# Performance work log

Hardware: AMD Instinct MI355X
Metric: run time of the kernel (lower is better)

## Reference

```python
import jax, jax.numpy as jnp
import numpy as np

N = 10000        # nodes
E = 640000       # edges (before self-loops)
IN = 128         # in_channels
HID = 32         # hidden_channels
HEADS = 4
HC = HID * HEADS # 128
OUT = 40         # out_channels
NEG_SLOPE = 0.2  # PyG GATConv default


def setup_inputs() -> dict:
    key = jax.random.key(0)
    ks = jax.random.split(key, 12)
    g = lambda k, shape: (jax.random.normal(k, shape, jnp.float32) * 0.1)
    return {
        "x": jax.random.normal(ks[0], (N, IN), jnp.float32),
        "edge_index": jax.random.randint(ks[1], (2, E), 0, N, dtype=jnp.int32),
        # conv1: in -> HID per head, HEADS heads, concat
        "W1": g(ks[2], (IN, HEADS * HID)),
        "a_src1": g(ks[3], (HEADS, HID)),
        "a_dst1": g(ks[4], (HEADS, HID)),
        "b1": jnp.zeros((HEADS * HID,), jnp.float32),
        # conv2: HC -> HC, 1 head
        "W2": g(ks[5], (HC, HC)),
        "a_src2": g(ks[6], (1, HC)),
        "a_dst2": g(ks[7], (1, HC)),
        "b2": jnp.zeros((HC,), jnp.float32),
        # final linear head
        "Wlin": g(ks[8], (HC, OUT)),
        "blin": jnp.zeros((OUT,), jnp.float32),
    }


def _gat_layer(x, W, a_src, a_dst, b, src, dst, heads, n):
    """PyG-style GATConv: gather -> edge attention -> segment softmax -> scatter."""
    d = W.shape[1] // heads
    h = (x @ W).reshape(n, heads, d)                       # [N, H, d]
    asrc = jnp.einsum('nhd,hd->nh', h, a_src)              # [N, H]
    adst = jnp.einsum('nhd,hd->nh', h, a_dst)
    e = jax.nn.leaky_relu(asrc[src] + adst[dst], NEG_SLOPE)  # [E, H]
    m = jax.ops.segment_max(e, dst, num_segments=n)          # per-dst max (stable softmax)
    p = jnp.exp(e - m[dst])
    z = jax.ops.segment_sum(p, dst, num_segments=n)
    alpha = p / (z[dst] + 1e-16)                             # [E, H]
    out = jax.ops.segment_sum(h[src] * alpha[:, :, None], dst, num_segments=n)
    return out.reshape(n, heads * d) + b


def reference(x, edge_index, W1, a_src1, a_dst1, b1, W2, a_src2, a_dst2, b2, Wlin, blin):
    n = x.shape[0]
    loop = jnp.arange(n, dtype=edge_index.dtype)           # add_self_loops=True
    src = jnp.concatenate([edge_index[0], loop])
    dst = jnp.concatenate([edge_index[1], loop])
    # eval mode: dropout is identity
    h1 = jax.nn.elu(_gat_layer(x, W1, a_src1, a_dst1, b1, src, dst, HEADS, n))
    h2 = jax.nn.elu(_gat_layer(h1, W2, a_src2, a_dst2, b2, src, dst, 1, n))
    return h2 @ Wlin + blin
```

## Files before the change

kernel.cpp:

```cpp
#include <hip/hip_runtime.h>
#include <hip/hip_bf16.h>

#define KSUB 8
#define SUBCAP 32
#define CAP 256

using bf16x8 = __attribute__((ext_vector_type(8))) short;
using f32x4  = __attribute__((ext_vector_type(4))) float;

static __device__ __forceinline__ short f2b(float f) {
    __hip_bfloat16 h = __float2bfloat16(f);
    return *reinterpret_cast<short*>(&h);
}
static __device__ __forceinline__ float blo(unsigned u) { return __uint_as_float(u << 16); }
static __device__ __forceinline__ float bhi(unsigned u) { return __uint_as_float(u & 0xffff0000u); }

__global__ void build_csr(const int* __restrict__ srcArr, const int* __restrict__ dstArr,
                          int E, int N, int* __restrict__ deg2,
                          unsigned short* __restrict__ csr) {
    int tid = threadIdx.x;
    int k_sub = blockIdx.x & (KSUB - 1);
    int Etot = E + N;
    int base = blockIdx.x * 1024 + tid;
#pragma unroll
    for (int k = 0; k < 4; k++) {
        int i = base + k * 256;
        if (i < Etot) {
            int s, d;
            if (i < E) { s = srcArr[i]; d = dstArr[i]; }
            else       { s = d = i - E; }
            int p = atomicAdd(&deg2[d * KSUB + k_sub], 1);
            if (p < SUBCAP) csr[d * CAP + k_sub * SUBCAP + p] = (unsigned short)s;
        }
    }
}

__global__ __launch_bounds__(256) void prep_w(const float* __restrict__ W1,
                                              const float* __restrict__ W2,
                                              short* __restrict__ Wt1,
                                              short* __restrict__ Wt2) {
    __shared__ float t[32][33];
    int which = blockIdx.x >> 4;
    int tile = blockIdx.x & 15;
    int bi = tile >> 2, bj = tile & 3;
    const float* W = which ? W2 : W1;
    short* Wt = which ? Wt2 : Wt1;
    int tx = threadIdx.x & 31, ty = threadIdx.x >> 5;
#pragma unroll
    for (int i = 0; i < 4; i++) {
        int r = bi * 32 + ty + 8 * i;
        t[ty + 8 * i][tx] = W[r * 128 + bj * 32 + tx];
    }
    __syncthreads();
#pragma unroll
    for (int i = 0; i < 4; i++) {
        int j = bj * 32 + ty + 8 * i;
        Wt[j * 128 + bi * 32 + tx] = f2b(t[tx][ty + 8 * i]);
    }
}

template <int H>
__global__ __launch_bounds__(256) void gemm_mfma(const float* __restrict__ x,
                        const short* __restrict__ Wt,
                        const float* __restrict__ a_src, const float* __restrict__ a_dst,
                        __hip_bfloat16* __restrict__ hwb, float* __restrict__ asrc,
                        float* __restrict__ adst, int N) {
    int wave = (blockIdx.x * 256 + threadIdx.x) >> 6;
    int lane = threadIdx.x & 63;
    int n0 = wave * 16;
    if (n0 >= N) return;
    int m = lane & 15, q = lane >> 4;
    int row = n0 + m;
    bf16x8 afrag[4];
    const float* xr = x + (size_t)row * 128 + q * 8;
#pragma unroll
    for (int kt = 0; kt < 4; kt++) {
        float4 v0 = *(const float4*)(xr + kt * 32);
        float4 v1 = *(const float4*)(xr + kt * 32 + 4);
        bf16x8 f;
        f[0] = f2b(v0.x); f[1] = f2b(v0.y); f[2] = f2b(v0.z); f[3] = f2b(v0.w);
        f[4] = f2b(v1.x); f[5] = f2b(v1.y); f[6] = f2b(v1.z); f[7] = f2b(v1.w);
        afrag[kt] = f;
    }
    float vs[4] = {0.f, 0.f, 0.f, 0.f}, vd[4] = {0.f, 0.f, 0.f, 0.f};
#pragma unroll
    for (int ct = 0; ct < 8; ct++) {
        f32x4 acc = {0.f, 0.f, 0.f, 0.f};
        const short* wrow = Wt + (ct * 16 + m) * 128 + q * 8;
#pragma unroll
        for (int kt = 0; kt < 4; kt++) {
            bf16x8 bfrag = *(const bf16x8*)(wrow + kt * 32);
            acc = __builtin_amdgcn_mfma_f32_16x16x32_bf16(afrag[kt], bfrag, acc, 0, 0, 0);
        }
        int col = ct * 16 + m;
        float asv = a_src[col], adv = a_dst[col];
#pragma unroll
        for (int r = 0; r < 4; r++) {
            int rr = n0 + q * 4 + r;
            hwb[rr * 128 + col] = __float2bfloat16(acc[r]);
            vs[r] += acc[r] * asv;
            vd[r] += acc[r] * adv;
        }
        if (H == 4 && (ct & 1) == 1) {
#pragma unroll
            for (int r = 0; r < 4; r++) {
                float a = vs[r], d = vd[r];
                for (int off = 8; off >= 1; off >>= 1) {
                    a += __shfl_xor(a, off); d += __shfl_xor(d, off);
                }
                if (m == 0) {
                    int rr = n0 + q * 4 + r;
                    asrc[rr * 4 + (ct >> 1)] = a;
                    adst[rr * 4 + (ct >> 1)] = d;
                }
                vs[r] = 0.f; vd[r] = 0.f;
            }
        }
    }
    if (H == 1) {
#pragma unroll
        for (int r = 0; r < 4; r++) {
            float a = vs[r], d = vd[r];
            for (int off = 8; off >= 1; off >>= 1) {
                a += __shfl_xor(a, off); d += __shfl_xor(d, off);
            }
            if (m == 0) {
                int rr = n0 + q * 4 + r;
                asrc[rr] = a;
                adst[rr] = d;
            }
        }
    }
}

__device__ __forceinline__ int slot8(int idx, const int* pref) {
    int k = 0;
#pragma unroll
    for (int j = 1; j < KSUB; j++) k += (idx >= pref[j]);
    return k * SUBCAP + (idx - pref[k]);
}

__global__ __launch_bounds__(64) void agg4(const __hip_bfloat16* __restrict__ hw,
                     const float* __restrict__ asrc, const float* __restrict__ adst,
                     const int* __restrict__ deg2, const unsigned short* __restrict__ csr_src,
                     const float* __restrict__ b, float* __restrict__ y, int N) {
    int n = blockIdx.x;
    int t = threadIdx.x;
    int er = t >> 4;
    int cg = t & 15;
    int hcol = cg >> 2;
    const int4* dp = (const int4*)&deg2[n * KSUB];
    int4 ca = dp[0], cb2 = dp[1];
    int pref[KSUB];
    int cnts[KSUB] = { min(ca.x,SUBCAP), min(ca.y,SUBCAP), min(ca.z,SUBCAP), min(ca.w,SUBCAP),
                       min(cb2.x,SUBCAP), min(cb2.y,SUBCAP), min(cb2.z,SUBCAP), min(cb2.w,SUBCAP) };
    pref[0] = 0;
#pragma unroll
    for (int k = 1; k < KSUB; k++) pref[k] = pref[k-1] + cnts[k-1];
    int deg = pref[KSUB-1] + cnts[KSUB-1];
    const uint4* hw4 = (const uint4*)hw;
    __shared__ float pe[128 * 4];
    __shared__ int se[128];
    float4 adl = *(const float4*)&adst[n * 4];
    float acc[8] = {0.f,0.f,0.f,0.f,0.f,0.f,0.f,0.f};
    float z0 = 0.f, z1 = 0.f, z2 = 0.f, z3 = 0.f;
    for (int base = 0; base < deg; base += 128) {
        int cnt = min(128, deg - base);
        __syncthreads();
#pragma unroll
        for (int rep = 0; rep < 2; rep++) {
            int idx = t + 64 * rep;
            if (idx < cnt) {
                int s = (int)csr_src[n * CAP + slot8(base + idx, pref)];
                se[idx] = s;
                float4 av = *(const float4*)&asrc[s * 4];
                float e0 = av.x + adl.x, e1 = av.y + adl.y;
                float e2 = av.z + adl.z, e3 = av.w + adl.w;
                e0 = e0 > 0.f ? e0 : 0.2f * e0;
                e1 = e1 > 0.f ? e1 : 0.2f * e1;
                e2 = e2 > 0.f ? e2 : 0.2f * e2;
                e3 = e3 > 0.f ? e3 : 0.2f * e3;
                float p0 = __expf(e0), p1 = __expf(e1), p2 = __expf(e2), p3 = __expf(e3);
                pe[idx * 4 + 0] = p0; pe[idx * 4 + 1] = p1;
                pe[idx * 4 + 2] = p2; pe[idx * 4 + 3] = p3;
                z0 += p0; z1 += p1; z2 += p2; z3 += p3;
            }
        }
        __syncthreads();
        for (int c = er; c < cnt; c += 4) {
            int s = se[c];
            float p = pe[c * 4 + hcol];
            uint4 v = hw4[s * 16 + cg];
            acc[0] += p * blo(v.x); acc[1] += p * bhi(v.x);
            acc[2] += p * blo(v.y); acc[3] += p * bhi(v.y);
            acc[4] += p * blo(v.z); acc[5] += p * bhi(v.z);
            acc[6] += p * blo(v.w); acc[7] += p * bhi(v.w);
        }
    }
#pragma unroll
    for (int i = 0; i < 8; i++) {
        acc[i] += __shfl_xor(acc[i], 16);
        acc[i] += __shfl_xor(acc[i], 32);
    }
    for (int off = 32; off >= 1; off >>= 1) {
        z0 += __shfl_xor(z0, off); z1 += __shfl_xor(z1, off);
        z2 += __shfl_xor(z2, off); z3 += __shfl_xor(z3, off);
    }
    float z = (hcol == 0) ? z0 : (hcol == 1) ? z1 : (hcol == 2) ? z2 : z3;
    float inv = 1.f / (z + 1e-16f);
    int col = cg * 8 + er * 2;
    float2 bb = *(const float2*)&b[col];
    float r0 = acc[er * 2]     * inv + bb.x;
    float r1 = acc[er * 2 + 1] * inv + bb.y;
    r0 = r0 > 0.f ? r0 : (__expf(r0) - 1.0f);
    r1 = r1 > 0.f ? r1 : (__expf(r1) - 1.0f);
    *(float2*)&y[n * 128 + col] = make_float2(r0, r1);
}

__global__ __launch_bounds__(64) void agg1_lin(const __hip_bfloat16* __restrict__ hw,
                         const float* __restrict__ asrc, const float* __restrict__ adst,
                         const int* __restrict__ deg2, const unsigned short* __restrict__ csr_src,
                         const float* __restrict__ b, const float* __restrict__ Wl,
                         const float* __restrict__ bl, float* __restrict__ out,
                         int N, int OUTC) {
    int n = blockIdx.x;
    int t = threadIdx.x;
    int er = t >> 4;
    int cg = t & 15;
    const int4* dp = (const int4*)&deg2[n * KSUB];
    int4 ca = dp[0], cb2 = dp[1];
    int pref[KSUB];
    int cnts[KSUB] = { min(ca.x,SUBCAP), min(ca.y,SUBCAP), min(ca.z,SUBCAP), min(ca.w,SUBCAP),
                       min(cb2.x,SUBCAP), min(cb2.y,SUBCAP), min(cb2.z,SUBCAP), min(cb2.w,SUBCAP) };
    pref[0] = 0;
#pragma unroll
    for (int k = 1; k < KSUB; k++) pref[k] = pref[k-1] + cnts[k-1];
    int deg = pref[KSUB-1] + cnts[KSUB-1];
    const uint4* hw4 = (const uint4*)hw;
    __shared__ float pe[128];
    __shared__ int se[128];
    __shared__ float yrow[128];
    float adl = adst[n];
    float acc[8] = {0.f,0.f,0.f,0.f,0.f,0.f,0.f,0.f};
    float zp = 0.f;
    for (int base = 0; base < deg; base += 128) {
        int cnt = min(128, deg - base);
        __syncthreads();
#pragma unroll
        for (int rep = 0; rep < 2; rep++) {
            int idx = t + 64 * rep;
            if (idx < cnt) {
                int s = (int)csr_src[n * CAP + slot8(base + idx, pref)];
                se[idx] = s;
                float e = asrc[s] + adl;
                e = e > 0.f ? e : 0.2f * e;
                float p = __expf(e);
                pe[idx] = p;
                zp += p;
            }
        }
        __syncthreads();
        for (int c = er; c < cnt; c += 4) {
            int s = se[c];
            float p = pe[c];
            uint4 v = hw4[s * 16 + cg];
            acc[0] += p * blo(v.x); acc[1] += p * bhi(v.x);
            acc[2] += p * blo(v.y); acc[3] += p * bhi(v.y);
            acc[4] += p * blo(v.z); acc[5] += p * bhi(v.z);
            acc[6] += p * blo(v.w); acc[7] += p * bhi(v.w);
        }
    }
#pragma unroll
    for (int i = 0; i < 8; i++) {
        acc[i] += __shfl_xor(acc[i], 16);
        acc[i] += __shfl_xor(acc[i], 32);
    }
    for (int off = 32; off >= 1; off >>= 1) zp += __shfl_xor(zp, off);
    float inv = 1.f / (zp + 1e-16f);
    int col = cg * 8 + er * 2;
    float2 bb = *(const float2*)&b[col];
    float r0 = acc[er * 2]     * inv + bb.x;
    float r1 = acc[er * 2 + 1] * inv + bb.y;
    r0 = r0 > 0.f ? r0 : (__expf(r0) - 1.0f);
    r1 = r1 > 0.f ? r1 : (__expf(r1) - 1.0f);
    yrow[col] = r0; yrow[col + 1] = r1;
    __syncthreads();
    if (t < OUTC) {
        float a = bl[t];
        for (int k = 0; k < 128; k++) a += yrow[k] * Wl[k * OUTC + t];
        out[n * OUTC + t] = a;
    }
}

extern "C" void kernel_launch(void* const* d_in, const int* in_sizes, int n_in,
                              void* d_out, int out_size, void* d_ws, size_t ws_size,
                              hipStream_t stream) {
    const float* x       = (const float*)d_in[0];
    const int*   ei      = (const int*)d_in[1];
    const float* W1      = (const float*)d_in[2];
    const float* a_src1  = (const float*)d_in[3];
    const float* a_dst1  = (const float*)d_in[4];
    const float* b1      = (const float*)d_in[5];
    const float* W2      = (const float*)d_in[6];
    const float* a_src2  = (const float*)d_in[7];
    const float* a_dst2  = (const float*)d_in[8];
    const float* b2      = (const float*)d_in[9];
    const float* Wlin    = (const float*)d_in[10];
    const float* blin    = (const float*)d_in[11];
    float* out = (float*)d_out;

    const int N = in_sizes[0] / 128;
    const int E = in_sizes[1] / 2;
    const int OUTC = in_sizes[10] / 128;
    const int Etot = E + N;
    const int* src = ei;
    const int* dst = ei + E;
    const int NCB = (Etot + 1023) / 1024;
    const int NGB = (N / 16 + 3) / 4;

    char* w = (char*)d_ws;
    size_t off = 0;
    auto alloc = [&](size_t bytes) -> char* {
        char* p = w + off;
        off += (bytes + 255) & ~(size_t)255;
        return p;
    };
    int*             deg2  = (int*)alloc((size_t)N * KSUB * 4);
    unsigned short*  csr   = (unsigned short*)alloc((size_t)N * CAP * 2);
    __hip_bfloat16*  hwb   = (__hip_bfloat16*)alloc((size_t)N * 128 * 2);
    float*           bufY  = (float*)alloc((size_t)N * 128 * 4);
    short*           Wt1   = (short*)alloc((size_t)128 * 128 * 2);
    short*           Wt2   = (short*)alloc((size_t)128 * 128 * 2);
    float*           asrc1 = (float*)alloc((size_t)N * 4 * 4);
    float*           adst1 = (float*)alloc((size_t)N * 4 * 4);
    float*           asrc2 = (float*)alloc((size_t)N * 4);
    float*           adst2 = (float*)alloc((size_t)N * 4);
    (void)ws_size;

    hipMemsetAsync(deg2, 0, (size_t)N * KSUB * 4, stream);
    prep_w<<<32, 256, 0, stream>>>(W1, W2, Wt1, Wt2);
    build_csr<<<NCB, 256, 0, stream>>>(src, dst, E, N, deg2, csr);

    gemm_mfma<4><<<NGB, 256, 0, stream>>>(x, Wt1, a_src1, a_dst1, hwb, asrc1, adst1, N);
    agg4<<<N, 64, 0, stream>>>(hwb, asrc1, adst1, deg2, csr, b1, bufY, N);

    gemm_mfma<1><<<NGB, 256, 0, stream>>>(bufY, Wt2, a_src2, a_dst2, hwb, asrc2, adst2, N);
    agg1_lin<<<N, 64, 0, stream>>>(hwb, asrc2, adst2, deg2, csr, b2, Wlin, blin, out, N, OUTC);
}
```

Before: 172.2 us.

## Fuse whole GAT pipeline into one cooperative persistent kernel with grid syncs

Replaces the memset plus six kernel launches with a single cooperative persistent kernel. Phases (weight prep, CSR build and first GEMM, layer-1 aggregation, second GEMM, layer-2 aggregation with the linear head) are separated by grid-wide syncs, and each wave processes nodes in a grid-stride loop with per-wave shared buffers. The aim is to remove launch gaps and tail effects between stages. The cost is grid.sync overhead, a grid limited by occupancy, and some loss of the block-per-node scheduling the aggregation kernels used. If the cooperative launch fails, it falls back to the original multi-kernel path.

```diff
diff --git a/kernel.cpp b/kernel.cpp
--- a/kernel.cpp
+++ b/kernel.cpp
@@ -1,9 +1,13 @@
 #include <hip/hip_runtime.h>
 #include <hip/hip_bf16.h>
+#include <hip/hip_cooperative_groups.h>
+
+namespace cg = cooperative_groups;
 
 #define KSUB 8
 #define SUBCAP 32
 #define CAP 256
+#define NTHR 256
 
 using bf16x8 = __attribute__((ext_vector_type(8))) short;
 using f32x4  = __attribute__((ext_vector_type(4))) float;
@@ -15,60 +19,20 @@
 static __device__ __forceinline__ float blo(unsigned u) { return __uint_as_float(u << 16); }
 static __device__ __forceinline__ float bhi(unsigned u) { return __uint_as_float(u & 0xffff0000u); }
 
-__global__ void build_csr(const int* __restrict__ srcArr, const int* __restrict__ dstArr,
-                          int E, int N, int* __restrict__ deg2,
-                          unsigned short* __restrict__ csr) {
-    int tid = threadIdx.x;
-    int k_sub = blockIdx.x & (KSUB - 1);
-    int Etot = E + N;
-    int base = blockIdx.x * 1024 + tid;
-#pragma unroll
-    for (int k = 0; k < 4; k++) {
-        int i = base + k * 256;
-        if (i < Etot) {
-            int s, d;
-            if (i < E) { s = srcArr[i]; d = dstArr[i]; }
-            else       { s = d = i - E; }
-            int p = atomicAdd(&deg2[d * KSUB + k_sub], 1);
-            if (p < SUBCAP) csr[d * CAP + k_sub * SUBCAP + p] = (unsigned short)s;
-        }
-    }
-}
-
-__global__ __launch_bounds__(256) void prep_w(const float* __restrict__ W1,
-                                              const float* __restrict__ W2,
-                                              short* __restrict__ Wt1,
-                                              short* __restrict__ Wt2) {
-    __shared__ float t[32][33];
-    int which = blockIdx.x >> 4;
-    int tile = blockIdx.x & 15;
-    int bi = tile >> 2, bj = tile & 3;
-    const float* W = which ? W2 : W1;
-    short* Wt = which ? Wt2 : Wt1;
-    int tx = threadIdx.x & 31, ty = threadIdx.x >> 5;
-#pragma unroll
-    for (int i = 0; i < 4; i++) {
-        int r = bi * 32 + ty + 8 * i;
-        t[ty + 8 * i][tx] = W[r * 128 + bj * 32 + tx];
-    }
-    __syncthreads();
-#pragma unroll
-    for (int i = 0; i < 4; i++) {
-        int j = bj * 32 + ty + 8 * i;
-        Wt[j * 128 + bi * 32 + tx] = f2b(t[tx][ty + 8 * i]);
-    }
+__device__ __forceinline__ int slot8(int idx, const int* pref) {
+    int k = 0;
+#pragma unroll
+    for (int j = 1; j < KSUB; j++) k += (idx >= pref[j]);
+    return k * SUBCAP + (idx - pref[k]);
 }
 
 template <int H>
-__global__ __launch_bounds__(256) void gemm_mfma(const float* __restrict__ x,
-                        const short* __restrict__ Wt,
-                        const float* __restrict__ a_src, const float* __restrict__ a_dst,
-                        __hip_bfloat16* __restrict__ hwb, float* __restrict__ asrc,
-                        float* __restrict__ adst, int N) {
-    int wave = (blockIdx.x * 256 + threadIdx.x) >> 6;
-    int lane = threadIdx.x & 63;
-    int n0 = wave * 16;
-    if (n0 >= N) return;
+__device__ void gemm_strip(int strip, int lane, const float* __restrict__ x,
+                           const short* __restrict__ Wt,
+                           const float* __restrict__ a_src, const float* __restrict__ a_dst,
+                           __hip_bfloat16* __restrict__ hwb, float* __restrict__ asrc,
+                           float* __restrict__ adst) {
+    int n0 = strip * 16;
     int m = lane & 15, q = lane >> 4;
     int row = n0 + m;
     bf16x8 afrag[4];
@@ -82,7 +46,7 @@
         f[4] = f2b(v1.x); f[5] = f2b(v1.y); f[6] = f2b(v1.z); f[7] = f2b(v1.w);
         afrag[kt] = f;
     }
-    float vs[4] = {0.f, 0.f, 0.f, 0.f}, vd[4] = {0.f, 0.f, 0.f, 0.f};
+    float vs[4] = {0.f,0.f,0.f,0.f}, vd[4] = {0.f,0.f,0.f,0.f};
 #pragma unroll
     for (int ct = 0; ct < 8; ct++) {
         f32x4 acc = {0.f, 0.f, 0.f, 0.f};
@@ -133,22 +97,69 @@
     }
 }
 
-__device__ __forceinline__ int slot8(int idx, const int* pref) {
-    int k = 0;
-#pragma unroll
-    for (int j = 1; j < KSUB; j++) k += (idx >= pref[j]);
-    return k * SUBCAP + (idx - pref[k]);
-}
-
-__global__ __launch_bounds__(64) void agg4(const __hip_bfloat16* __restrict__ hw,
+__global__ void k_build_csr(const int* __restrict__ srcArr, const int* __restrict__ dstArr,
+                            int E, int N, int* __restrict__ deg2,
+                            unsigned short* __restrict__ csr) {
+    int tid = threadIdx.x;
+    int k_sub = blockIdx.x & (KSUB - 1);
+    int Etot = E + N;
+    int base = blockIdx.x * 1024 + tid;
+#pragma unroll
+    for (int k = 0; k < 4; k++) {
+        int i = base + k * 256;
+        if (i < Etot) {
+            int s, d;
+            if (i < E) { s = srcArr[i]; d = dstArr[i]; }
+            else       { s = d = i - E; }
+            int p = atomicAdd(&deg2[d * KSUB + k_sub], 1);
+            if (p < SUBCAP) csr[d * CAP + k_sub * SUBCAP + p] = (unsigned short)s;
+        }
+    }
+}
+
+__global__ __launch_bounds__(256) void k_prep_w(const float* __restrict__ W1,
+                                                const float* __restrict__ W2,
+                                                short* __restrict__ Wt1,
+                                                short* __restrict__ Wt2) {
+    __shared__ float t[32][33];
+    int which = blockIdx.x >> 4;
+    int tile = blockIdx.x & 15;
+    int bi = tile >> 2, bj = tile & 3;
+    const float* W = which ? W2 : W1;
+    short* Wt = which ? Wt2 : Wt1;
+    int tx = threadIdx.x & 31, ty = threadIdx.x >> 5;
+#pragma unroll
+    for (int i = 0; i < 4; i++) {
+        int r = bi * 32 + ty + 8 * i;
+        t[ty + 8 * i][tx] = W[r * 128 + bj * 32 + tx];
+    }
+    __syncthreads();
+#pragma unroll
+    for (int i = 0; i < 4; i++) {
+        int j = bj * 32 + ty + 8 * i;
+        Wt[j * 128 + bi * 32 + tx] = f2b(t[tx][ty + 8 * i]);
+    }
+}
+
+template <int H>
+__global__ __launch_bounds__(256) void k_gemm_mfma(const float* __restrict__ x,
+                        const short* __restrict__ Wt,
+                        const float* __restrict__ a_src, const float* __restrict__ a_dst,
+                        __hip_bfloat16* __restrict__ hwb, float* __restrict__ asrc,
+                        float* __restrict__ adst, int N) {
+    int wave = (blockIdx.x * 256 + threadIdx.x) >> 6;
+    int lane = threadIdx.x & 63;
+    if (wave * 16 >= N) return;
+    gemm_strip<H>(wave, lane, x, Wt, a_src, a_dst, hwb, asrc, adst);
+}
+
+__global__ __launch_bounds__(64) void k_agg4(const __hip_bfloat16* __restrict__ hw,
                      const float* __restrict__ asrc, const float* __restrict__ adst,
                      const int* __restrict__ deg2, const unsigned short* __restrict__ csr_src,
                      const float* __restrict__ b, float* __restrict__ y, int N) {
     int n = blockIdx.x;
     int t = threadIdx.x;
-    int er = t >> 4;
-    int cg = t & 15;
-    int hcol = cg >> 2;
+    int er = t >> 4, cgp = t & 15, hcol = cgp >> 2;
     const int4* dp = (const int4*)&deg2[n * KSUB];
     int4 ca = dp[0], cb2 = dp[1];
     int pref[KSUB];
@@ -159,7 +170,7 @@
     for (int k = 1; k < KSUB; k++) pref[k] = pref[k-1] + cnts[k-1];
     int deg = pref[KSUB-1] + cnts[KSUB-1];
     const uint4* hw4 = (const uint4*)hw;
-    __shared__ float pe[128 * 4];
+    __shared__ float pe[512];
     __shared__ int se[128];
     float4 adl = *(const float4*)&adst[n * 4];
     float acc[8] = {0.f,0.f,0.f,0.f,0.f,0.f,0.f,0.f};
@@ -190,7 +201,7 @@
         for (int c = er; c < cnt; c += 4) {
             int s = se[c];
             float p = pe[c * 4 + hcol];
-            uint4 v = hw4[s * 16 + cg];
+            uint4 v = hw4[s * 16 + cgp];
             acc[0] += p * blo(v.x); acc[1] += p * bhi(v.x);
             acc[2] += p * blo(v.y); acc[3] += p * bhi(v.y);
             acc[4] += p * blo(v.z); acc[5] += p * bhi(v.z);
@@ -208,7 +219,7 @@
     }
     float z = (hcol == 0) ? z0 : (hcol == 1) ? z1 : (hcol == 2) ? z2 : z3;
     float inv = 1.f / (z + 1e-16f);
-    int col = cg * 8 + er * 2;
+    int col = cgp * 8 + er * 2;
     float2 bb = *(const float2*)&b[col];
     float r0 = acc[er * 2]     * inv + bb.x;
     float r1 = acc[er * 2 + 1] * inv + bb.y;
@@ -217,7 +228,7 @@
     *(float2*)&y[n * 128 + col] = make_float2(r0, r1);
 }
 
-__global__ __launch_bounds__(64) void agg1_lin(const __hip_bfloat16* __restrict__ hw,
+__global__ __launch_bounds__(64) void k_agg1_lin(const __hip_bfloat16* __restrict__ hw,
                          const float* __restrict__ asrc, const float* __restrict__ adst,
                          const int* __restrict__ deg2, const unsigned short* __restrict__ csr_src,
                          const float* __restrict__ b, const float* __restrict__ Wl,
@@ -225,8 +236,7 @@
                          int N, int OUTC) {
     int n = blockIdx.x;
     int t = threadIdx.x;
-    int er = t >> 4;
-    int cg = t & 15;
+    int er = t >> 4, cgp = t & 15;
     const int4* dp = (const int4*)&deg2[n * KSUB];
     int4 ca = dp[0], cb2 = dp[1];
     int pref[KSUB];
@@ -263,7 +273,7 @@
         for (int c = er; c < cnt; c += 4) {
             int s = se[c];
             float p = pe[c];
-            uint4 v = hw4[s * 16 + cg];
+            uint4 v = hw4[s * 16 + cgp];
             acc[0] += p * blo(v.x); acc[1] += p * bhi(v.x);
             acc[2] += p * blo(v.y); acc[3] += p * bhi(v.y);
             acc[4] += p * blo(v.z); acc[5] += p * bhi(v.z);
@@ -277,7 +287,7 @@
     }
     for (int off = 32; off >= 1; off >>= 1) zp += __shfl_xor(zp, off);
     float inv = 1.f / (zp + 1e-16f);
-    int col = cg * 8 + er * 2;
+    int col = cgp * 8 + er * 2;
     float2 bb = *(const float2*)&b[col];
     float r0 = acc[er * 2]     * inv + bb.x;
     float r1 = acc[er * 2 + 1] * inv + bb.y;
@@ -292,31 +302,224 @@
     }
 }
 
+struct MegaArgs {
+    const int* src; const int* dst; int E; int N;
+    const float* x;
+    const float* W1; const float* W2;
+    const float* a_src1; const float* a_dst1; const float* b1;
+    const float* a_src2; const float* a_dst2; const float* b2;
+    const float* Wlin; const float* blin; float* out; int OUTC;
+    int* deg2; unsigned short* csr; __hip_bfloat16* hwb; float* bufY;
+    short* Wt1; short* Wt2;
+    float* asrc1; float* adst1; float* asrc2; float* adst2;
+};
+
+union SmemU {
+    float prep[32][33];
+    struct { float pe[4][512]; int se[4][128]; } a4;
+    struct { float pe[4][128]; int se[4][128]; float yrow[4][128]; } a1;
+};
+
+__global__ __launch_bounds__(NTHR) void mega(MegaArgs A) {
+    cg::grid_group grid = cg::this_grid();
+    __shared__ SmemU sm;
+    const int tid  = threadIdx.x;
+    const int lane = tid & 63;
+    const int wv   = tid >> 6;
+    const int gwave = blockIdx.x * 4 + wv;
+    const int gtid  = blockIdx.x * NTHR + tid;
+    const int totw  = gridDim.x * 4;
+    const int tott  = gridDim.x * NTHR;
+    const int N = A.N, E = A.E, Etot = A.E + A.N;
+
+    for (int i = gtid; i < N * KSUB; i += tott) A.deg2[i] = 0;
+    if (blockIdx.x < 32) {
+        int which = blockIdx.x >> 4;
+        int tile = blockIdx.x & 15;
+        int bi = tile >> 2, bj = tile & 3;
+        const float* W = which ? A.W2 : A.W1;
+        short* Wt = which ? A.Wt2 : A.Wt1;
+        int tx = tid & 31, ty = tid >> 5;
+#pragma unroll
+        for (int i = 0; i < 4; i++) {
+            int r = bi * 32 + ty + 8 * i;
+            sm.prep[ty + 8 * i][tx] = W[r * 128 + bj * 32 + tx];
+        }
+        __syncthreads();
+#pragma unroll
+        for (int i = 0; i < 4; i++) {
+            int j = bj * 32 + ty + 8 * i;
+            Wt[j * 128 + bi * 32 + tx] = f2b(sm.prep[tx][ty + 8 * i]);
+        }
+    }
+    __threadfence();
+    grid.sync();
+
+    for (int strip = gwave; strip < N / 16; strip += totw)
+        gemm_strip<4>(strip, lane, A.x, A.Wt1, A.a_src1, A.a_dst1, A.hwb, A.asrc1, A.adst1);
+    for (int i = gtid; i < Etot; i += tott) {
+        int s, d;
+        if (i < E) { s = A.src[i]; d = A.dst[i]; }
+        else       { s = d = i - E; }
+        int k_sub = (i >> 10) & (KSUB - 1);
+        int p = atomicAdd(&A.deg2[d * KSUB + k_sub], 1);
+        if (p < SUBCAP) A.csr[d * CAP + k_sub * SUBCAP + p] = (unsigned short)s;
+    }
+    __threadfence();
+    grid.sync();
+
+    {
+        int er = lane >> 4, cgp = lane & 15, hcol = cgp >> 2;
+        const uint4* hw4 = (const uint4*)A.hwb;
+        float* pew = sm.a4.pe[wv];
+        int*   sew = sm.a4.se[wv];
+        for (int n = gwave; n < N; n += totw) {
+            const int4* dp = (const int4*)&A.deg2[n * KSUB];
+            int4 ca = dp[0], cb2 = dp[1];
+            int pref[KSUB];
+            int cnts[KSUB] = { min(ca.x,SUBCAP), min(ca.y,SUBCAP), min(ca.z,SUBCAP), min(ca.w,SUBCAP),
+                               min(cb2.x,SUBCAP), min(cb2.y,SUBCAP), min(cb2.z,SUBCAP), min(cb2.w,SUBCAP) };
+            pref[0] = 0;
+#pragma unroll
+            for (int k = 1; k < KSUB; k++) pref[k] = pref[k-1] + cnts[k-1];
+            int deg = pref[KSUB-1] + cnts[KSUB-1];
+            float4 adl = *(const float4*)&A.adst1[n * 4];
+            float acc[8] = {0.f,0.f,0.f,0.f,0.f,0.f,0.f,0.f};
+            float z0 = 0.f, z1 = 0.f, z2 = 0.f, z3 = 0.f;
+            for (int base = 0; base < deg; base += 128) {
+                int cnt = min(128, deg - base);
+#pragma unroll
+                for (int rep = 0; rep < 2; rep++) {
+                    int idx = lane + 64 * rep;
+                    if (idx < cnt) {
+                        int s = (int)A.csr[n * CAP + slot8(base + idx, pref)];
+                        sew[idx] = s;
+                        float4 av = *(const float4*)&A.asrc1[s * 4];
+                        float e0 = av.x + adl.x, e1 = av.y + adl.y;
+                        float e2 = av.z + adl.z, e3 = av.w + adl.w;
+                        e0 = e0 > 0.f ? e0 : 0.2f * e0;
+                        e1 = e1 > 0.f ? e1 : 0.2f * e1;
+                        e2 = e2 > 0.f ? e2 : 0.2f * e2;
+                        e3 = e3 > 0.f ? e3 : 0.2f * e3;
+                        float p0 = __expf(e0), p1 = __expf(e1), p2 = __expf(e2), p3 = __expf(e3);
+                        pew[idx * 4 + 0] = p0; pew[idx * 4 + 1] = p1;
+                        pew[idx * 4 + 2] = p2; pew[idx * 4 + 3] = p3;
+                        z0 += p0; z1 += p1; z2 += p2; z3 += p3;
+                    }
+                }
+                for (int c = er; c < cnt; c += 4) {
+                    int s = sew[c];
+                    float p = pew[c * 4 + hcol];
+                    uint4 v = hw4[s * 16 + cgp];
+                    acc[0] += p * blo(v.x); acc[1] += p * bhi(v.x);
+                    acc[2] += p * blo(v.y); acc[3] += p * bhi(v.y);
+                    acc[4] += p * blo(v.z); acc[5] += p * bhi(v.z);
+                    acc[6] += p * blo(v.w); acc[7] += p * bhi(v.w);
+                }
+            }
+#pragma unroll
+            for (int i = 0; i < 8; i++) {
+                acc[i] += __shfl_xor(acc[i], 16);
+                acc[i] += __shfl_xor(acc[i], 32);
+            }
+            for (int off = 32; off >= 1; off >>= 1) {
+                z0 += __shfl_xor(z0, off); z1 += __shfl_xor(z1, off);
+                z2 += __shfl_xor(z2, off); z3 += __shfl_xor(z3, off);
+            }
+            float z = (hcol == 0) ? z0 : (hcol == 1) ? z1 : (hcol == 2) ? z2 : z3;
+            float inv = 1.f / (z + 1e-16f);
+            int col = cgp * 8 + er * 2;
+            float2 bb = *(const float2*)&A.b1[col];
+            float r0 = acc[er * 2]     * inv + bb.x;
+            float r1 = acc[er * 2 + 1] * inv + bb.y;
+            r0 = r0 > 0.f ? r0 : (__expf(r0) - 1.0f);
+            r1 = r1 > 0.f ? r1 : (__expf(r1) - 1.0f);
+            *(float2*)&A.bufY[n * 128 + col] = make_float2(r0, r1);
+        }
+    }
+    __threadfence();
+    grid.sync();
+
+    for (int strip = gwave; strip < N / 16; strip += totw)
+        gemm_strip<1>(strip, lane, A.bufY, A.Wt2, A.a_src2, A.a_dst2, A.hwb, A.asrc2, A.adst2);
+    __threadfence();
+    grid.sync();
+
+    {
+        int er = lane >> 4, cgp = lane & 15;
+        const uint4* hw4 = (const uint4*)A.hwb;
+        float* pew = sm.a1.pe[wv];
+        int*   sew = sm.a1.se[wv];
+        float* yr  = sm.a1.yrow[wv];
+        for (int n = gwave; n < N; n += totw) {
+            const int4* dp = (const int4*)&A.deg2[n * KSUB];
+            int4 ca = dp[0], cb2 = dp[1];
+            int pref[KSUB];
+            int cnts[KSUB] = { min(ca.x,SUBCAP), min(ca.y,SUBCAP), min(ca.z,SUBCAP), min(ca.w,SUBCAP),
+                               min(cb2.x,SUBCAP), min(cb2.y,SUBCAP), min(cb2.z,SUBCAP), min(cb2.w,SUBCAP) };
+            pref[0] = 0;
+#pragma unroll
+            for (int k = 1; k < KSUB; k++) pref[k] = pref[k-1] + cnts[k-1];
+            int deg = pref[KSUB-1] + cnts[KSUB-1];
+            float adl = A.adst2[n];
+            float acc[8] = {0.f,0.f,0.f,0.f,0.f,0.f,0.f,0.f};
+            float zp = 0.f;
+            for (int base = 0; base < deg; base += 128) {
+                int cnt = min(128, deg - base);
+#pragma unroll
+                for (int rep = 0; rep < 2; rep++) {
+                    int idx = lane + 64 * rep;
+                    if (idx < cnt) {
+                        int s = (int)A.csr[n * CAP + slot8(base + idx, pref)];
+                        sew[idx] = s;
+                        float e = A.asrc2[s] + adl;
+                        e = e > 0.f ? e : 0.2f * e;
+                        float p = __expf(e);
+                        pew[idx] = p;
+                        zp += p;
+                    }
+                }
+                for (int c = er; c < cnt; c += 4) {
+                    int s = sew[c];
+                    float p = pew[c];
+                    uint4 v = hw4[s * 16 + cgp];
+                    acc[0] += p * blo(v.x); acc[1] += p * bhi(v.x);
+                    acc[2] += p * blo(v.y); acc[3] += p * bhi(v.y);
+                    acc[4] += p * blo(v.z); acc[5] += p * bhi(v.z);
+                    acc[6] += p * blo(v.w); acc[7] += p * bhi(v.w);
+                }
+            }
+#pragma unroll
+            for (int i = 0; i < 8; i++) {
+                acc[i] += __shfl_xor(acc[i], 16);
+                acc[i] += __shfl_xor(acc[i], 32);
+            }
+            for (int off = 32; off >= 1; off >>= 1) zp += __shfl_xor(zp, off);
+            float inv = 1.f / (zp + 1e-16f);
+            int col = cgp * 8 + er * 2;
+            float2 bb = *(const float2*)&A.b2[col];
+            float r0 = acc[er * 2]     * inv + bb.x;
+            float r1 = acc[er * 2 + 1] * inv + bb.y;
+            r0 = r0 > 0.f ? r0 : (__expf(r0) - 1.0f);
+            r1 = r1 > 0.f ? r1 : (__expf(r1) - 1.0f);
+            yr[col] = r0; yr[col + 1] = r1;
+            if (lane < A.OUTC) {
+                float a = A.blin[lane];
+                for (int k = 0; k < 128; k++) a += yr[k] * A.Wlin[k * A.OUTC + lane];
+                A.out[n * A.OUTC + lane] = a;
+            }
+        }
+    }
+}
+
 extern "C" void kernel_launch(void* const* d_in, const int* in_sizes, int n_in,
                               void* d_out, int out_size, void* d_ws, size_t ws_size,
                               hipStream_t stream) {
-    const float* x       = (const float*)d_in[0];
-    const int*   ei      = (const int*)d_in[1];
-    const float* W1      = (const float*)d_in[2];
-    const float* a_src1  = (const float*)d_in[3];
-    const float* a_dst1  = (const float*)d_in[4];
-    const float* b1      = (const float*)d_in[5];
-    const float* W2      = (const float*)d_in[6];
-    const float* a_src2  = (const float*)d_in[7];
-    const float* a_dst2  = (const float*)d_in[8];
-    const float* b2      = (const float*)d_in[9];
-    const float* Wlin    = (const float*)d_in[10];
-    const float* blin    = (const float*)d_in[11];
-    float* out = (float*)d_out;
-
     const int N = in_sizes[0] / 128;
     const int E = in_sizes[1] / 2;
     const int OUTC = in_sizes[10] / 128;
     const int Etot = E + N;
-    const int* src = ei;
-    const int* dst = ei + E;
-    const int NCB = (Etot + 1023) / 1024;
-    const int NGB = (N / 16 + 3) / 4;
+    const int* ei = (const int*)d_in[1];
 
     char* w = (char*)d_ws;
     size_t off = 0;
@@ -325,25 +528,55 @@
         off += (bytes + 255) & ~(size_t)255;
         return p;
     };
-    int*             deg2  = (int*)alloc((size_t)N * KSUB * 4);
-    unsigned short*  csr   = (unsigned short*)alloc((size_t)N * CAP * 2);
-    __hip_bfloat16*  hwb   = (__hip_bfloat16*)alloc((size_t)N * 128 * 2);
-    float*           bufY  = (float*)alloc((size_t)N * 128 * 4);
-    short*           Wt1   = (short*)alloc((size_t)128 * 128 * 2);
-    short*           Wt2   = (short*)alloc((size_t)128 * 128 * 2);
-    float*           asrc1 = (float*)alloc((size_t)N * 4 * 4);
-    float*           adst1 = (float*)alloc((size_t)N * 4 * 4);
-    float*           asrc2 = (float*)alloc((size_t)N * 4);
-    float*           adst2 = (float*)alloc((size_t)N * 4);
+    MegaArgs A;
+    A.src = ei; A.dst = ei + E; A.E = E; A.N = N;
+    A.x      = (const float*)d_in[0];
+    A.W1     = (const float*)d_in[2];
+    A.a_src1 = (const float*)d_in[3];
+    A.a_dst1 = (const float*)d_in[4];
+    A.b1     = (const float*)d_in[5];
+    A.W2     = (const float*)d_in[6];
+    A.a_src2 = (const float*)d_in[7];
+    A.a_dst2 = (const float*)d_in[8];
+    A.b2     = (const float*)d_in[9];
+    A.Wlin   = (const float*)d_in[10];
+    A.blin   = (const float*)d_in[11];
+    A.out    = (float*)d_out;
+    A.OUTC   = OUTC;
+    A.deg2  = (int*)alloc((size_t)N * KSUB * 4);
+    A.csr   = (unsigned short*)alloc((size_t)N * CAP * 2);
+    A.hwb   = (__hip_bfloat16*)alloc((size_t)N * 128 * 2);
+    A.bufY  = (float*)alloc((size_t)N * 128 * 4);
+    A.Wt1   = (short*)alloc((size_t)128 * 128 * 2);
+    A.Wt2   = (short*)alloc((size_t)128 * 128 * 2);
+    A.asrc1 = (float*)alloc((size_t)N * 4 * 4);
+    A.adst1 = (float*)alloc((size_t)N * 4 * 4);
+    A.asrc2 = (float*)alloc((size_t)N * 4);
+    A.adst2 = (float*)alloc((size_t)N * 4);
     (void)ws_size;
 
-    hipMemsetAsync(deg2, 0, (size_t)N * KSUB * 4, stream);
-    prep_w<<<32, 256, 0, stream>>>(W1, W2, Wt1, Wt2);
-    build_csr<<<NCB, 256, 0, stream>>>(src, dst, E, N, deg2, csr);
-
-    gemm_mfma<4><<<NGB, 256, 0, stream>>>(x, Wt1, a_src1, a_dst1, hwb, asrc1, adst1, N);
-    agg4<<<N, 64, 0, stream>>>(hwb, asrc1, adst1, deg2, csr, b1, bufY, N);
-
-    gemm_mfma<1><<<NGB, 256, 0, stream>>>(bufY, Wt2, a_src2, a_dst2, hwb, asrc2, adst2, N);
-    agg1_lin<<<N, 64, 0, stream>>>(hwb, asrc2, adst2, deg2, csr, b2, Wlin, blin, out, N, OUTC);
-}
+    int maxBlk = 0;
+    hipError_t qrc = hipOccupancyMaxActiveBlocksPerMultiprocessor(&maxBlk, mega, NTHR, 0);
+    hipError_t lrc = hipErrorUnknown;
+    if (qrc == hipSuccess && maxBlk > 0) {
+        int nblk = maxBlk * 256;
+        if (nblk > 2048) nblk = 2048;
+        void* args[] = { &A };
+        lrc = hipLaunchCooperativeKernel((const void*)mega, dim3(nblk), dim3(NTHR),
+                                         args, 0, stream);
+    }
+    if (lrc == hipSuccess) return;
+
+    const int NCB = (Etot + 1023) / 1024;
+    const int NGB = (N / 16 + 3) / 4;
+    hipMemsetAsync(A.deg2, 0, (size_t)N * KSUB * 4, stream);
+    k_prep_w<<<32, 256, 0, stream>>>(A.W1, A.W2, A.Wt1, A.Wt2);
+    k_build_csr<<<NCB, 256, 0, stream>>>(A.src, A.dst, E, N, A.deg2, A.csr);
+    k_gemm_mfma<4><<<NGB, 256, 0, stream>>>(A.x, A.Wt1, A.a_src1, A.a_dst1,
+                                            A.hwb, A.asrc1, A.adst1, N);
+    k_agg4<<<N, 64, 0, stream>>>(A.hwb, A.asrc1, A.adst1, A.deg2, A.csr, A.b1, A.bufY, N);
+    k_gemm_mfma<1><<<NGB, 256, 0, stream>>>(A.bufY, A.Wt2, A.a_src2, A.a_dst2,
+                                            A.hwb, A.asrc2, A.adst2, N);
+    k_agg1_lin<<<N, 64, 0, stream>>>(A.hwb, A.asrc2, A.adst2, A.deg2, A.csr, A.b2,
+                                     A.Wlin, A.blin, A.out, N, OUTC);
+}
```

Measured after the change: 500.5 us. 191% more time.
